# Performance work log

Measured on AMD Instinct MI355X. Metric: run time of the kernel, lower is better.

Reference implementation:

```python
import jax, jax.numpy as jnp
import numpy as np

N, E, ENC, EMB, PI = 100000, 1600000, 128, 128, 98
ALPHA1, ALPHA2 = 0.5, 0.5


def setup_inputs() -> dict:
    key = jax.random.key(0)
    ks = jax.random.split(key, 20)
    s = 0.05
    return {
        "x": jax.random.normal(ks[0], (N, ENC), jnp.float32),
        "d2an": jax.random.normal(ks[1], (N, PI), jnp.float32),
        "ei0": jax.random.randint(ks[2], (2, E), 0, N, jnp.int32),
        "ew0": jax.random.uniform(ks[3], (E,), jnp.float32, 0.1, 4.0),
        "ei1": jax.random.randint(ks[4], (2, E), 0, N, jnp.int32),
        "ew1": jax.random.uniform(ks[5], (E,), jnp.float32, 0.1, 4.0),
        "nodeW1": jax.random.normal(ks[6], (ENC, ENC + PI), jnp.float32) * s,
        "nodeW2": jax.random.normal(ks[7], (ENC, ENC + PI), jnp.float32) * s,
        "W1a": jax.random.normal(ks[8], (EMB, ENC), jnp.float32) * s,
        "W1b": jax.random.normal(ks[9], (EMB, ENC), jnp.float32) * s,
        "W2a": jax.random.normal(ks[10], (EMB, ENC), jnp.float32) * s,
        "W2b": jax.random.normal(ks[11], (EMB, ENC), jnp.float32) * s,
        "W3a": jax.random.normal(ks[12], (EMB, EMB), jnp.float32) * s,
        "W3b": jax.random.normal(ks[13], (EMB, EMB), jnp.float32) * s,
        "W4a": jax.random.normal(ks[14], (EMB, EMB), jnp.float32) * s,
        "W4b": jax.random.normal(ks[15], (EMB, EMB), jnp.float32) * s,
    }


def _layer(x, ei, ew, W1, W2, nodeW, d2an, first):
    """PosKnnGNNLayer.forward: add self loops, optional nodeLin, GCN deg norm +
    edge norm, gather -> lin1/lin2 -> scale -> scatter-add (aggr='add')."""
    n = x.shape[0]
    loop = jnp.arange(n, dtype=ei.dtype)
    row = jnp.concatenate([ei[0], loop])          # source nodes (x_j)
    col = jnp.concatenate([ei[1], loop])          # target nodes (aggregation)
    attr = jnp.concatenate([ew, jnp.ones((n,), ew.dtype)])  # self-loop fill=1.0
    if first:
        x = jnp.concatenate([x, d2an], axis=1) @ nodeW.T
    deg = jax.ops.segment_sum(jnp.ones_like(attr), col, num_segments=n)
    dis = jnp.where(deg > 0, jax.lax.rsqrt(jnp.maximum(deg, 1.0)), 0.0)
    deg_norm = dis[row] * dis[col]                # [E']
    einv = attr ** -0.5
    einv = jnp.where(jnp.isinf(einv), 0.0, einv)
    einv = jnp.minimum(einv, 1.0)                 # clamp >1 to 1
    h1 = x @ W1.T                                 # [N, out]
    h2 = x @ W2.T
    msg = deg_norm[:, None] * h1[row] + einv[:, None] * h2[row]  # [E', out]
    return jax.ops.segment_sum(msg, col, num_segments=n)


def reference(x, d2an, ei0, ew0, ei1, ew1, nodeW1, nodeW2,
              W1a, W1b, W2a, W2b, W3a, W3b, W4a, W4b):
    # eval mode: dropout(p=0.3) is identity
    x0 = jax.nn.relu(_layer(x, ei0, ew0, W1a, W1b, nodeW1, d2an, True))
    x1 = jax.nn.relu(_layer(x, ei1, ew1, W2a, W2b, nodeW2, d2an, True))
    xm = ALPHA1 * x0 + ALPHA2 * x1
    x0 = jax.nn.relu(_layer(xm, ei0, ew0, W3a, W3b, None, None, False))
    x1 = jax.nn.relu(_layer(xm, ei1, ew1, W4a, W4b, None, None, False))
    return ALPHA1 * x0 + ALPHA2 * x1
```

## Files before the change

kernel.cpp:

```cpp
#include <hip/hip_runtime.h>
#include <hip/hip_fp16.h>
#include <stdint.h>

#define NN 100000
#define NE 1600000
#define ETOT (NE + NN)
#define EPB 8192
#define NBLK ((NE + EPB - 1) / EPB)
#define NPB 512
#define NBUK ((NN + NPB - 1) / NPB)

typedef __attribute__((ext_vector_type(8))) short bf16x8;
typedef __attribute__((ext_vector_type(4))) float f32x4;
typedef __attribute__((ext_vector_type(4))) unsigned short us4;

__device__ __forceinline__ float bf2f(unsigned short u) {
    union { unsigned int i; float f; } x; x.i = ((unsigned int)u) << 16; return x.f;
}
__device__ __forceinline__ unsigned short f2bf(float f) {
    union { float f; unsigned int i; } x; x.f = f;
    unsigned int i = x.i;
    return (unsigned short)((i + 0x7FFFu + ((i >> 16) & 1u)) >> 16);
}
__device__ __forceinline__ int packab(float a, float b) {
    unsigned int ua = __half_as_ushort(__float2half_rn(a));
    unsigned int ub = __half_as_ushort(__float2half_rn(b));
    return (int)(ua | (ub << 16));
}
__device__ __forceinline__ float2 unpackab(int p) {
    float a = __half2float(__ushort_as_half((unsigned short)(p & 0xFFFF)));
    float b = __half2float(__ushort_as_half((unsigned short)(((unsigned int)p) >> 16)));
    return make_float2(a, b);
}

__global__ void k_init_deg(int* deg0, int* deg1) {
    int i = blockIdx.x * 256 + threadIdx.x;
    if (i < NN) { deg0[i] = 1; deg1[i] = 1; }
}

__global__ void k_count(const int* col0, const int* col1, int* deg0, int* deg1) {
    int t = blockIdx.x * 256 + threadIdx.x;
    if (t * 4 >= NE) return;
    const int* col = blockIdx.y ? col1 : col0;
    int* deg = blockIdx.y ? deg1 : deg0;
    int4 a = ((const int4*)col)[t];
    atomicAdd(&deg[a.x], 1); atomicAdd(&deg[a.y], 1);
    atomicAdd(&deg[a.z], 1); atomicAdd(&deg[a.w], 1);
}

__global__ void k_scan1(const int* deg0, const int* deg1, int* rp0, int* rp1s, int* bsum) {
    __shared__ int s[256];
    const int* deg = blockIdx.y ? deg1 : deg0;
    int* rp = (blockIdx.y ? rp1s : rp0) + 1;
    int* bs = bsum + blockIdx.y * 128;
    int tid = threadIdx.x;
    int base = blockIdx.x * 1024 + tid * 4;
    int v0 = 0, v1 = 0, v2 = 0, v3 = 0;
    if (base + 0 < NN) v0 = deg[base + 0];
    if (base + 1 < NN) v1 = deg[base + 1];
    if (base + 2 < NN) v2 = deg[base + 2];
    if (base + 3 < NN) v3 = deg[base + 3];
    int sum = v0 + v1 + v2 + v3;
    s[tid] = sum; __syncthreads();
    for (int off = 1; off < 256; off <<= 1) {
        int t = (tid >= off) ? s[tid - off] : 0;
        __syncthreads(); s[tid] += t; __syncthreads();
    }
    int run = s[tid] - sum;
    if (base + 0 < NN) { run += v0; rp[base + 0] = run; }
    if (base + 1 < NN) { run += v1; rp[base + 1] = run; }
    if (base + 2 < NN) { run += v2; rp[base + 2] = run; }
    if (base + 3 < NN) { run += v3; rp[base + 3] = run; }
    if (tid == 255) bs[blockIdx.x] = s[255];
}

__global__ void k_scan2(int* bsum, int nb) {
    __shared__ int s[128];
    int* bs = bsum + blockIdx.x * 128;
    int tid = threadIdx.x;
    int v = (tid < nb) ? bs[tid] : 0;
    s[tid] = v; __syncthreads();
    for (int off = 1; off < 128; off <<= 1) {
        int t = (tid >= off) ? s[tid - off] : 0;
        __syncthreads(); s[tid] += t; __syncthreads();
    }
    if (tid < nb) bs[tid] = s[tid] - v;
}

__global__ void k_scan3(int* rp0, int* rp1s, const int* bsum) {
    int* rowptr = blockIdx.y ? rp1s : rp0;
    int add = bsum[blockIdx.y * 128 + blockIdx.x];
    int tid = threadIdx.x;
    int base = blockIdx.x * 1024 + tid * 4;
    #pragma unroll
    for (int i = 0; i < 4; i++) {
        int idx = base + i;
        if (idx < NN) rowptr[idx + 1] += add;
    }
    if (blockIdx.x == 0 && tid == 0) rowptr[0] = 0;
}

__global__ void k_self(const int* rp0, const int* rp1s, const int* deg0, const int* deg1,
                       int2* eo0, int2* eo1, float* dis0, float* dis1) {
    int i = blockIdx.x * 256 + threadIdx.x;
    if (i >= NN) return;
    const int* rowptr = blockIdx.y ? rp1s : rp0;
    const int* deg = blockIdx.y ? deg1 : deg0;
    int2* eo = blockIdx.y ? eo1 : eo0;
    float* dis = blockIdx.y ? dis1 : dis0;
    int p = rowptr[i];
    float d = (float)deg[i];
    eo[p] = make_int2(i, packab(1.0f / d, 1.0f));
    dis[i] = rsqrtf(d);
}

__global__ __launch_bounds__(256) void k_cnt(const int* ei0, const int* ei1, int* cntm) {
    __shared__ int h[NBUK];
    const int* col = (blockIdx.y ? ei1 : ei0) + NE;
    for (int i = threadIdx.x; i < NBUK; i += 256) h[i] = 0;
    __syncthreads();
    int base = blockIdx.x * EPB;
    for (int i = 0; i < EPB / 256; i++) {
        int e = base + i * 256 + threadIdx.x;
        if (e < NE) atomicAdd(&h[col[e] >> 9], 1);
    }
    __syncthreads();
    int* out = cntm + ((size_t)blockIdx.y * NBLK + blockIdx.x) * NBUK;
    for (int i = threadIdx.x; i < NBUK; i += 256) out[i] = h[i];
}

__global__ __launch_bounds__(256) void k_base(const int* rp0, const int* rp1s,
                                              const int* cntm, int* basem, int* btot) {
    __shared__ int s[256];
    int b = blockIdx.x;
    const int* rowptr = blockIdx.y ? rp1s : rp0;
    const int* cnt = cntm + (size_t)blockIdx.y * NBLK * NBUK;
    int t = threadIdx.x;
    int v = (t < NBLK) ? cnt[(size_t)t * NBUK + b] : 0;
    s[t] = v; __syncthreads();
    for (int off = 1; off < 256; off <<= 1) {
        int u = (t >= off) ? s[t - off] : 0;
        __syncthreads(); s[t] += u; __syncthreads();
    }
    int excl = s[t] - v;
    int base0 = rowptr[b * NPB];
    if (t < NBLK) basem[((size_t)blockIdx.y * NBLK + t) * NBUK + b] = base0 + excl;
    if (t == 255) btot[blockIdx.y * NBUK + b] = s[255];
}

__global__ __launch_bounds__(256) void k_scat1(const int* ei0, const float* ew0,
                                               const int* ei1, const float* ew1,
                                               const float* dis0, const float* dis1,
                                               const int* basem, int2* st0, int2* st1) {
    __shared__ int lb[NBUK];
    __shared__ int lc[NBUK];
    const int* er = blockIdx.y ? ei1 : ei0;
    const float* ew = blockIdx.y ? ew1 : ew0;
    const float* dis = blockIdx.y ? dis1 : dis0;
    int2* st = blockIdx.y ? st1 : st0;
    const int* bm = basem + ((size_t)blockIdx.y * NBLK + blockIdx.x) * NBUK;
    for (int i = threadIdx.x; i < NBUK; i += 256) { lb[i] = bm[i]; lc[i] = 0; }
    __syncthreads();
    int base = blockIdx.x * EPB;
    for (int i = 0; i < EPB / 256; i++) {
        int e = base + i * 256 + threadIdx.x;
        if (e >= NE) break;
        int r = er[e];
        int c = er[NE + e];
        int bkt = c >> 9;
        int rank = atomicAdd(&lc[bkt], 1);
        float a = dis[r] * dis[c];
        float b = fminf(rsqrtf(ew[e]), 1.0f);
        st[lb[bkt] + rank] = make_int2(r | ((c & 511) << 17), packab(a, b));
    }
}

__global__ __launch_bounds__(256) void k_scat2(const int* rp0, const int* rp1s,
                                               const int* btot,
                                               const int2* st0, const int2* st1,
                                               int2* eo0, int2* eo1) {
    __shared__ int lcur[NPB];
    int b = blockIdx.x;
    const int* rowptr = blockIdx.y ? rp1s : rp0;
    const int2* st = blockIdx.y ? st1 : st0;
    int2* eo = blockIdx.y ? eo1 : eo0;
    int nstart = b * NPB;
    for (int i = threadIdx.x; i < NPB; i += 256) {
        int node = nstart + i;
        if (node < NN) lcur[i] = rowptr[node] + 1;
    }
    __syncthreads();
    int s0 = rowptr[nstart];
    int tot = btot[blockIdx.y * NBUK + b];
    for (int j = s0 + (int)threadIdx.x; j < s0 + tot; j += 256) {
        int2 rec = st[j];
        int cl = (rec.x >> 17) & 511;
        int pos = atomicAdd(&lcur[cl], 1);
        eo[pos] = make_int2(rec.x & 0x1FFFF, rec.y);
    }
}

__global__ void k_packx(const float* x, const float* d2, unsigned short* Xc) {
    int idx = blockIdx.x * 256 + threadIdx.x;
    if (idx >= NN * 64) return;
    int r = idx >> 6, k4 = (idx & 63) << 2;
    us4 o;
    if (k4 < 128) {
        float4 v = *(const float4*)(x + (size_t)r * 128 + k4);
        o[0] = f2bf(v.x); o[1] = f2bf(v.y); o[2] = f2bf(v.z); o[3] = f2bf(v.w);
    } else {
        #pragma unroll
        for (int i = 0; i < 4; i++) {
            int k = k4 + i;
            float v = (k < 226) ? d2[(size_t)r * 98 + (k - 128)] : 0.f;
            o[i] = f2bf(v);
        }
    }
    *(us4*)(Xc + (size_t)r * 256 + k4) = o;
}

__global__ void k_packw(const float* wn1, const float* wn2,
                        const float* w1a, const float* w1b,
                        const float* w2a, const float* w2b,
                        const float* w3a, const float* w3b,
                        const float* w4a, const float* w4b,
                        unsigned short* Wfnode, unsigned short* WfL) {
    int idx = blockIdx.x * 256 + threadIdx.x;
    if (idx < 65536) {
        int j = idx & 7, lane = (idx >> 3) & 63, ct = (idx >> 9) & 15, ks = idx >> 13;
        int k = ks * 32 + (lane >> 4) * 8 + j;
        int c = ct * 16 + (lane & 15);
        float v = 0.f;
        if (k < 226) v = (c < 128) ? wn1[c * 226 + k] : wn2[(c - 128) * 226 + k];
        Wfnode[idx] = f2bf(v);
    } else if (idx < 196608) {
        int li = idx - 65536;
        int set = li >> 15, r = li & 32767;
        const float* wa = (set == 0) ? w1a : (set == 1) ? w2a : (set == 2) ? w3a : w4a;
        const float* wb = (set == 0) ? w1b : (set == 1) ? w2b : (set == 2) ? w3b : w4b;
        int j = r & 7, lane = (r >> 3) & 63, ct = (r >> 9) & 7, ks = r >> 12;
        int k = ks * 32 + (lane >> 4) * 8 + j;
        int c = ct * 16 + (lane & 15);
        float v = (k < 128) ? wa[c * 128 + k] : wb[c * 128 + (k - 128)];
        WfL[li] = f2bf(v);
    }
}

template <int SRST, int SOFF>
__global__ __launch_bounds__(256) void k_agg(const unsigned short* S,
                                             const int* rowptr, const int2* eg,
                                             unsigned short* G) {
    int c = blockIdx.x * 4 + (threadIdx.x >> 6);
    int lane = threadIdx.x & 63;
    if (c >= NN) return;
    float a0 = 0.f, a1 = 0.f, b0 = 0.f, b1 = 0.f;
    int jb = rowptr[c], je = rowptr[c + 1];
    const unsigned short* Sb = S + SOFF + lane * 2;
    int j = jb;
    for (; j + 16 <= je; j += 16) {
        int2 e[16]; unsigned int u[16];
        #pragma unroll
        for (int i = 0; i < 16; i++) e[i] = eg[j + i];
        #pragma unroll
        for (int i = 0; i < 16; i++)
            u[i] = *(const unsigned int*)(Sb + (size_t)e[i].x * SRST);
        #pragma unroll
        for (int i = 0; i < 16; i++) {
            float2 w = unpackab(e[i].y);
            float x0 = bf2f((unsigned short)(u[i] & 0xFFFF));
            float x1 = bf2f((unsigned short)(u[i] >> 16));
            a0 += w.x * x0; a1 += w.x * x1; b0 += w.y * x0; b1 += w.y * x1;
        }
    }
    for (; j + 4 <= je; j += 4) {
        int2 e[4]; unsigned int u[4];
        #pragma unroll
        for (int i = 0; i < 4; i++) e[i] = eg[j + i];
        #pragma unroll
        for (int i = 0; i < 4; i++)
            u[i] = *(const unsigned int*)(Sb + (size_t)e[i].x * SRST);
        #pragma unroll
        for (int i = 0; i < 4; i++) {
            float2 w = unpackab(e[i].y);
            float x0 = bf2f((unsigned short)(u[i] & 0xFFFF));
            float x1 = bf2f((unsigned short)(u[i] >> 16));
            a0 += w.x * x0; a1 += w.x * x1; b0 += w.y * x0; b1 += w.y * x1;
        }
    }
    for (; j < je; j++) {
        int2 e = eg[j];
        unsigned int u = *(const unsigned int*)(Sb + (size_t)e.x * SRST);
        float2 w = unpackab(e.y);
        float x0 = bf2f((unsigned short)(u & 0xFFFF));
        float x1 = bf2f((unsigned short)(u >> 16));
        a0 += w.x * x0; a1 += w.x * x1; b0 += w.y * x0; b1 += w.y * x1;
    }
    unsigned int* gd = (unsigned int*)(G + (size_t)c * 256);
    gd[lane]      = (unsigned int)f2bf(a0) | ((unsigned int)f2bf(a1) << 16);
    gd[64 + lane] = (unsigned int)f2bf(b0) | ((unsigned int)f2bf(b1) << 16);
}

template <int MODE>
__global__ __launch_bounds__(256) void k_gemm(const unsigned short* A, int arst,
                                              const unsigned short* Wf, int nct_total,
                                              unsigned short* outB, float* outF,
                                              const unsigned short* T, int orst) {
    int wave = threadIdx.x >> 6, lane = threadIdx.x & 63;
    int m = lane & 15, quad = lane >> 4;
    int row0 = blockIdx.x * 64 + wave * 16;
    int arow = row0 + m;
    bool rowok = arow < NN;
    const unsigned short* Ap = A + (size_t)arow * arst + quad * 8;
    int ctbase = blockIdx.y * 8;
    f32x4 acc[8];
    #pragma unroll
    for (int t = 0; t < 8; t++) acc[t] = (f32x4){0.f, 0.f, 0.f, 0.f};

    #pragma unroll
    for (int ks = 0; ks < 8; ks++) {
        bf16x8 a;
        if (rowok) a = *(const bf16x8*)(Ap + ks * 32);
        else       a = (bf16x8){0, 0, 0, 0, 0, 0, 0, 0};
        const unsigned short* wp = Wf + ((size_t)(ks * nct_total + ctbase) * 64 + lane) * 8;
        #pragma unroll
        for (int t = 0; t < 8; t++) {
            bf16x8 b = *(const bf16x8*)(wp + t * 512);
            acc[t] = __builtin_amdgcn_mfma_f32_16x16x32_bf16(a, b, acc[t], 0, 0, 0);
        }
    }

    int col0 = blockIdx.y * 128;
    #pragma unroll
    for (int t = 0; t < 8; t++) {
        int c = col0 + t * 16 + m;
        #pragma unroll
        for (int rg = 0; rg < 4; rg++) {
            int r = row0 + quad * 4 + rg;
            if (r < NN) {
                float v = acc[t][rg];
                if (MODE == 0) {
                    outB[(size_t)r * orst + c] = f2bf(v);
                } else {
                    float tv = bf2f(T[(size_t)r * 128 + c]);
                    float o = 0.5f * fmaxf(tv, 0.f) + 0.5f * fmaxf(v, 0.f);
                    if (MODE == 1) outB[(size_t)r * orst + c] = f2bf(o);
                    else           outF[(size_t)r * 128 + c] = o;
                }
            }
        }
    }
}

extern "C" void kernel_launch(void* const* d_in, const int* in_sizes, int n_in,
                              void* d_out, int out_size, void* d_ws, size_t ws_size,
                              hipStream_t stream) {
    const float* x      = (const float*)d_in[0];
    const float* d2an   = (const float*)d_in[1];
    const int*   ei0    = (const int*)d_in[2];
    const float* ew0    = (const float*)d_in[3];
    const int*   ei1    = (const int*)d_in[4];
    const float* ew1    = (const float*)d_in[5];
    const float* nodeW1 = (const float*)d_in[6];
    const float* nodeW2 = (const float*)d_in[7];
    const float* W1a = (const float*)d_in[8],  *W1b = (const float*)d_in[9];
    const float* W2a = (const float*)d_in[10], *W2b = (const float*)d_in[11];
    const float* W3a = (const float*)d_in[12], *W3b = (const float*)d_in[13];
    const float* W4a = (const float*)d_in[14], *W4b = (const float*)d_in[15];
    float* out = (float*)d_out;

    char* p = (char*)d_ws;
    auto alloc = [&](size_t bytes) -> char* {
        char* r = p; p += (bytes + 255) & ~(size_t)255; return r;
    };
    unsigned short* bufA   = (unsigned short*)alloc((size_t)NN * 256 * 2);
    unsigned short* bufB   = (unsigned short*)alloc((size_t)NN * 256 * 2);
    unsigned short* Tbuf   = (unsigned short*)alloc((size_t)NN * 128 * 2);
    unsigned short* Wfnode = (unsigned short*)alloc(65536 * 2);
    unsigned short* WfL    = (unsigned short*)alloc((size_t)4 * 32768 * 2);
    int*    deg0    = (int*)alloc((size_t)NN * 4);
    int*    deg1    = (int*)alloc((size_t)NN * 4);
    int*    rowptr0 = (int*)alloc((size_t)(NN + 1) * 4);
    int*    rowptr1 = (int*)alloc((size_t)(NN + 1) * 4);
    int*    bsum    = (int*)alloc(2 * 128 * 4);
    float*  dis0    = (float*)alloc((size_t)NN * 4);
    float*  dis1    = (float*)alloc((size_t)NN * 4);
    int2*   eo0     = (int2*)alloc((size_t)ETOT * 8);
    int2*   eo1     = (int2*)alloc((size_t)ETOT * 8);
    int*    cntm    = (int*)alloc((size_t)2 * NBLK * NBUK * 4);
    int*    basem   = (int*)alloc((size_t)2 * NBLK * NBUK * 4);
    int*    btot    = (int*)alloc((size_t)2 * NBUK * 4);

    int2* st0 = (int2*)bufB;
    int2* st1 = st0 + ETOT;

    int nbN  = (NN + 255) / 256;
    int nbE4 = (NE / 4 + 255) / 256;
    int nbS  = (NN + 1023) / 1024;
    dim3 gP((NN + 63) / 64, 2);
    dim3 gL((NN + 63) / 64, 1);
    int nbA = (NN + 3) / 4;

    k_init_deg<<<nbN, 256, 0, stream>>>(deg0, deg1);
    k_count<<<dim3(nbE4, 2), 256, 0, stream>>>(ei0 + NE, ei1 + NE, deg0, deg1);
    k_scan1<<<dim3(nbS, 2), 256, 0, stream>>>(deg0, deg1, rowptr0, rowptr1, bsum);
    k_scan2<<<2, 128, 0, stream>>>(bsum, nbS);
    k_scan3<<<dim3(nbS, 2), 256, 0, stream>>>(rowptr0, rowptr1, bsum);
    k_self<<<dim3(nbN, 2), 256, 0, stream>>>(rowptr0, rowptr1, deg0, deg1,
                                             eo0, eo1, dis0, dis1);
    k_cnt<<<dim3(NBLK, 2), 256, 0, stream>>>(ei0, ei1, cntm);
    k_base<<<dim3(NBUK, 2), 256, 0, stream>>>(rowptr0, rowptr1, cntm, basem, btot);
    k_scat1<<<dim3(NBLK, 2), 256, 0, stream>>>(ei0, ew0, ei1, ew1,
                                               dis0, dis1, basem, st0, st1);
    k_scat2<<<dim3(NBUK, 2), 256, 0, stream>>>(rowptr0, rowptr1, btot,
                                               st0, st1, eo0, eo1);

    k_packx<<<(NN * 64 + 255) / 256, 256, 0, stream>>>(x, d2an, bufA);
    k_packw<<<768, 256, 0, stream>>>(nodeW1, nodeW2, W1a, W1b, W2a, W2b,
                                     W3a, W3b, W4a, W4b, Wfnode, WfL);

    k_gemm<0><<<gP, 256, 0, stream>>>(bufA, 256, Wfnode, 16, bufB, nullptr, nullptr, 256);
    k_agg<256, 0><<<nbA, 256, 0, stream>>>(bufB, rowptr0, eo0, bufA);
    k_gemm<0><<<gL, 256, 0, stream>>>(bufA, 256, WfL, 8, Tbuf, nullptr, nullptr, 128);
    k_agg<256, 128><<<nbA, 256, 0, stream>>>(bufB, rowptr1, eo1, bufA);
    k_gemm<1><<<gL, 256, 0, stream>>>(bufA, 256, WfL + 32768, 8, bufB, nullptr, Tbuf, 128);

    k_agg<128, 0><<<nbA, 256, 0, stream>>>(bufB, rowptr0, eo0, bufA);
    k_gemm<0><<<gL, 256, 0, stream>>>(bufA, 256, WfL + 2 * 32768, 8, Tbuf, nullptr, nullptr, 128);
    k_agg<128, 0><<<nbA, 256, 0, stream>>>(bufB, rowptr1, eo1, bufA);
    k_gemm<2><<<gL, 256, 0, stream>>>(bufA, 256, WfL + 3 * 32768, 8, nullptr, out, Tbuf, 128);
}
```

Measured before the change: 916.4 us.

## Compute degrees from bucketed edges instead of global atomics

Reorders CSR construction so edges are first bucket-scattered by target block, then per-bucket shared-memory histograms produce node degrees, removing the global atomicAdd degree count pass. Bucket offsets now come from a standalone bucket-total scan instead of rowptr. Edge normalisation (dis product and clamped rsqrt of weight) moves into the second scatter, using shared-memory dis for the target. This adds two small kernels and an extra read of the staged edges.

```diff
diff --git a/kernel.cpp b/kernel.cpp
--- a/kernel.cpp
+++ b/kernel.cpp
@@ -33,19 +33,97 @@
     return make_float2(a, b);
 }
 
-__global__ void k_init_deg(int* deg0, int* deg1) {
-    int i = blockIdx.x * 256 + threadIdx.x;
-    if (i < NN) { deg0[i] = 1; deg1[i] = 1; }
-}
-
-__global__ void k_count(const int* col0, const int* col1, int* deg0, int* deg1) {
-    int t = blockIdx.x * 256 + threadIdx.x;
-    if (t * 4 >= NE) return;
-    const int* col = blockIdx.y ? col1 : col0;
+__global__ __launch_bounds__(256) void k_cnt(const int* ei0, const int* ei1, int* cntm) {
+    __shared__ int h[NBUK];
+    const int* col = (blockIdx.y ? ei1 : ei0) + NE;
+    for (int i = threadIdx.x; i < NBUK; i += 256) h[i] = 0;
+    __syncthreads();
+    int base = blockIdx.x * EPB;
+    for (int i = 0; i < EPB / 256; i++) {
+        int e = base + i * 256 + threadIdx.x;
+        if (e < NE) atomicAdd(&h[col[e] >> 9], 1);
+    }
+    __syncthreads();
+    int* out = cntm + ((size_t)blockIdx.y * NBLK + blockIdx.x) * NBUK;
+    for (int i = threadIdx.x; i < NBUK; i += 256) out[i] = h[i];
+}
+
+__global__ __launch_bounds__(256) void k_btot(const int* cntm, int* bstart, int* btot) {
+    __shared__ int s[256];
+    int t = threadIdx.x;
+    const int* cnt = cntm + (size_t)blockIdx.y * NBLK * NBUK;
+    int tot = 0;
+    if (t < NBUK)
+        for (int blk = 0; blk < NBLK; blk++) tot += cnt[(size_t)blk * NBUK + t];
+    s[t] = tot; __syncthreads();
+    for (int off = 1; off < 256; off <<= 1) {
+        int u = (t >= off) ? s[t - off] : 0;
+        __syncthreads(); s[t] += u; __syncthreads();
+    }
+    if (t < NBUK) {
+        bstart[blockIdx.y * NBUK + t] = s[t] - tot;
+        btot[blockIdx.y * NBUK + t] = tot;
+    }
+}
+
+__global__ __launch_bounds__(256) void k_base2(const int* cntm, const int* bstart, int* basem) {
+    __shared__ int s[256];
+    int b = blockIdx.x;
+    const int* cnt = cntm + (size_t)blockIdx.y * NBLK * NBUK;
+    int t = threadIdx.x;
+    int v = (t < NBLK) ? cnt[(size_t)t * NBUK + b] : 0;
+    s[t] = v; __syncthreads();
+    for (int off = 1; off < 256; off <<= 1) {
+        int u = (t >= off) ? s[t - off] : 0;
+        __syncthreads(); s[t] += u; __syncthreads();
+    }
+    if (t < NBLK)
+        basem[((size_t)blockIdx.y * NBLK + t) * NBUK + b] =
+            bstart[blockIdx.y * NBUK + b] + (s[t] - v);
+}
+
+__global__ __launch_bounds__(256) void k_scat1(const int* ei0, const float* ew0,
+                                               const int* ei1, const float* ew1,
+                                               const int* basem, int2* st0, int2* st1) {
+    __shared__ int lb[NBUK];
+    __shared__ int lc[NBUK];
+    const int* er = blockIdx.y ? ei1 : ei0;
+    const float* ew = blockIdx.y ? ew1 : ew0;
+    int2* st = blockIdx.y ? st1 : st0;
+    const int* bm = basem + ((size_t)blockIdx.y * NBLK + blockIdx.x) * NBUK;
+    for (int i = threadIdx.x; i < NBUK; i += 256) { lb[i] = bm[i]; lc[i] = 0; }
+    __syncthreads();
+    int base = blockIdx.x * EPB;
+    for (int i = 0; i < EPB / 256; i++) {
+        int e = base + i * 256 + threadIdx.x;
+        if (e >= NE) break;
+        int r = er[e];
+        int c = er[NE + e];
+        float w = ew[e];
+        int bkt = c >> 9;
+        int rank = atomicAdd(&lc[bkt], 1);
+        st[lb[bkt] + rank] = make_int2(r | ((c & 511) << 17), __float_as_int(w));
+    }
+}
+
+__global__ __launch_bounds__(256) void k_deg(const int* bstart, const int* btot,
+                                             const int2* st0, const int2* st1,
+                                             int* deg0, int* deg1) {
+    __shared__ int h[NPB];
+    int b = blockIdx.x;
+    const int2* st = blockIdx.y ? st1 : st0;
     int* deg = blockIdx.y ? deg1 : deg0;
-    int4 a = ((const int4*)col)[t];
-    atomicAdd(&deg[a.x], 1); atomicAdd(&deg[a.y], 1);
-    atomicAdd(&deg[a.z], 1); atomicAdd(&deg[a.w], 1);
+    for (int i = threadIdx.x; i < NPB; i += 256) h[i] = 0;
+    __syncthreads();
+    int s0 = bstart[blockIdx.y * NBUK + b];
+    int tot = btot[blockIdx.y * NBUK + b];
+    for (int j = s0 + (int)threadIdx.x; j < s0 + tot; j += 256)
+        atomicAdd(&h[(st[j].x >> 17) & 511], 1);
+    __syncthreads();
+    for (int i = threadIdx.x; i < NPB; i += 256) {
+        int node = b * NPB + i;
+        if (node < NN) deg[node] = h[i] + 1;
+    }
 }
 
 __global__ void k_scan1(const int* deg0, const int* deg1, int* rp0, int* rp1s, int* bsum) {
@@ -114,89 +192,35 @@
     dis[i] = rsqrtf(d);
 }
 
-__global__ __launch_bounds__(256) void k_cnt(const int* ei0, const int* ei1, int* cntm) {
-    __shared__ int h[NBUK];
-    const int* col = (blockIdx.y ? ei1 : ei0) + NE;
-    for (int i = threadIdx.x; i < NBUK; i += 256) h[i] = 0;
-    __syncthreads();
-    int base = blockIdx.x * EPB;
-    for (int i = 0; i < EPB / 256; i++) {
-        int e = base + i * 256 + threadIdx.x;
-        if (e < NE) atomicAdd(&h[col[e] >> 9], 1);
-    }
-    __syncthreads();
-    int* out = cntm + ((size_t)blockIdx.y * NBLK + blockIdx.x) * NBUK;
-    for (int i = threadIdx.x; i < NBUK; i += 256) out[i] = h[i];
-}
-
-__global__ __launch_bounds__(256) void k_base(const int* rp0, const int* rp1s,
-                                              const int* cntm, int* basem, int* btot) {
-    __shared__ int s[256];
-    int b = blockIdx.x;
-    const int* rowptr = blockIdx.y ? rp1s : rp0;
-    const int* cnt = cntm + (size_t)blockIdx.y * NBLK * NBUK;
-    int t = threadIdx.x;
-    int v = (t < NBLK) ? cnt[(size_t)t * NBUK + b] : 0;
-    s[t] = v; __syncthreads();
-    for (int off = 1; off < 256; off <<= 1) {
-        int u = (t >= off) ? s[t - off] : 0;
-        __syncthreads(); s[t] += u; __syncthreads();
-    }
-    int excl = s[t] - v;
-    int base0 = rowptr[b * NPB];
-    if (t < NBLK) basem[((size_t)blockIdx.y * NBLK + t) * NBUK + b] = base0 + excl;
-    if (t == 255) btot[blockIdx.y * NBUK + b] = s[255];
-}
-
-__global__ __launch_bounds__(256) void k_scat1(const int* ei0, const float* ew0,
-                                               const int* ei1, const float* ew1,
+__global__ __launch_bounds__(256) void k_scat2(const int* rp0, const int* rp1s,
+                                               const int* bstart, const int* btot,
                                                const float* dis0, const float* dis1,
-                                               const int* basem, int2* st0, int2* st1) {
-    __shared__ int lb[NBUK];
-    __shared__ int lc[NBUK];
-    const int* er = blockIdx.y ? ei1 : ei0;
-    const float* ew = blockIdx.y ? ew1 : ew0;
-    const float* dis = blockIdx.y ? dis1 : dis0;
-    int2* st = blockIdx.y ? st1 : st0;
-    const int* bm = basem + ((size_t)blockIdx.y * NBLK + blockIdx.x) * NBUK;
-    for (int i = threadIdx.x; i < NBUK; i += 256) { lb[i] = bm[i]; lc[i] = 0; }
-    __syncthreads();
-    int base = blockIdx.x * EPB;
-    for (int i = 0; i < EPB / 256; i++) {
-        int e = base + i * 256 + threadIdx.x;
-        if (e >= NE) break;
-        int r = er[e];
-        int c = er[NE + e];
-        int bkt = c >> 9;
-        int rank = atomicAdd(&lc[bkt], 1);
-        float a = dis[r] * dis[c];
-        float b = fminf(rsqrtf(ew[e]), 1.0f);
-        st[lb[bkt] + rank] = make_int2(r | ((c & 511) << 17), packab(a, b));
-    }
-}
-
-__global__ __launch_bounds__(256) void k_scat2(const int* rp0, const int* rp1s,
-                                               const int* btot,
                                                const int2* st0, const int2* st1,
                                                int2* eo0, int2* eo1) {
     __shared__ int lcur[NPB];
+    __shared__ float ldis[NPB];
     int b = blockIdx.x;
     const int* rowptr = blockIdx.y ? rp1s : rp0;
+    const float* dis = blockIdx.y ? dis1 : dis0;
     const int2* st = blockIdx.y ? st1 : st0;
     int2* eo = blockIdx.y ? eo1 : eo0;
     int nstart = b * NPB;
     for (int i = threadIdx.x; i < NPB; i += 256) {
         int node = nstart + i;
-        if (node < NN) lcur[i] = rowptr[node] + 1;
-    }
-    __syncthreads();
-    int s0 = rowptr[nstart];
+        if (node < NN) { lcur[i] = rowptr[node] + 1; ldis[i] = dis[node]; }
+    }
+    __syncthreads();
+    int s0 = bstart[blockIdx.y * NBUK + b];
     int tot = btot[blockIdx.y * NBUK + b];
     for (int j = s0 + (int)threadIdx.x; j < s0 + tot; j += 256) {
         int2 rec = st[j];
         int cl = (rec.x >> 17) & 511;
+        int r  = rec.x & 0x1FFFF;
+        float w = __int_as_float(rec.y);
+        float a = dis[r] * ldis[cl];
+        float bb = fminf(rsqrtf(w), 1.0f);
         int pos = atomicAdd(&lcur[cl], 1);
-        eo[pos] = make_int2(rec.x & 0x1FFFF, rec.y);
+        eo[pos] = make_int2(r, packab(a, bb));
     }
 }
 
@@ -389,30 +413,29 @@
     int*    cntm    = (int*)alloc((size_t)2 * NBLK * NBUK * 4);
     int*    basem   = (int*)alloc((size_t)2 * NBLK * NBUK * 4);
     int*    btot    = (int*)alloc((size_t)2 * NBUK * 4);
+    int*    bstart  = (int*)alloc((size_t)2 * NBUK * 4);
 
     int2* st0 = (int2*)bufB;
-    int2* st1 = st0 + ETOT;
+    int2* st1 = st0 + NE;
 
     int nbN  = (NN + 255) / 256;
-    int nbE4 = (NE / 4 + 255) / 256;
     int nbS  = (NN + 1023) / 1024;
     dim3 gP((NN + 63) / 64, 2);
     dim3 gL((NN + 63) / 64, 1);
     int nbA = (NN + 3) / 4;
 
-    k_init_deg<<<nbN, 256, 0, stream>>>(deg0, deg1);
-    k_count<<<dim3(nbE4, 2), 256, 0, stream>>>(ei0 + NE, ei1 + NE, deg0, deg1);
+    k_cnt<<<dim3(NBLK, 2), 256, 0, stream>>>(ei0, ei1, cntm);
+    k_btot<<<dim3(1, 2), 256, 0, stream>>>(cntm, bstart, btot);
+    k_base2<<<dim3(NBUK, 2), 256, 0, stream>>>(cntm, bstart, basem);
+    k_scat1<<<dim3(NBLK, 2), 256, 0, stream>>>(ei0, ew0, ei1, ew1, basem, st0, st1);
+    k_deg<<<dim3(NBUK, 2), 256, 0, stream>>>(bstart, btot, st0, st1, deg0, deg1);
     k_scan1<<<dim3(nbS, 2), 256, 0, stream>>>(deg0, deg1, rowptr0, rowptr1, bsum);
     k_scan2<<<2, 128, 0, stream>>>(bsum, nbS);
     k_scan3<<<dim3(nbS, 2), 256, 0, stream>>>(rowptr0, rowptr1, bsum);
     k_self<<<dim3(nbN, 2), 256, 0, stream>>>(rowptr0, rowptr1, deg0, deg1,
                                              eo0, eo1, dis0, dis1);
-    k_cnt<<<dim3(NBLK, 2), 256, 0, stream>>>(ei0, ei1, cntm);
-    k_base<<<dim3(NBUK, 2), 256, 0, stream>>>(rowptr0, rowptr1, cntm, basem, btot);
-    k_scat1<<<dim3(NBLK, 2), 256, 0, stream>>>(ei0, ew0, ei1, ew1,
-                                               dis0, dis1, basem, st0, st1);
-    k_scat2<<<dim3(NBUK, 2), 256, 0, stream>>>(rowptr0, rowptr1, btot,
-                                               st0, st1, eo0, eo1);
+    k_scat2<<<dim3(NBUK, 2), 256, 0, stream>>>(rowptr0, rowptr1, bstart, btot,
+                                               dis0, dis1, st0, st1, eo0, eo1);
 
     k_packx<<<(NN * 64 + 255) / 256, 256, 0, stream>>>(x, d2an, bufA);
     k_packw<<<768, 256, 0, stream>>>(nodeW1, nodeW2, W1a, W1b, W2a, W2b,
```

Result: faster. 775.4 us (-15.4%).
